# Performance work log

Hardware: AMD Instinct MI355X
Metric: run time of the kernel (lower is better)

## Reference

```python
import jax, jax.numpy as jnp
import numpy as np

N, E, R, D_IN, D_OUT = 50000, 800000, 8, 64, 64


def setup_inputs() -> dict:
    key = jax.random.key(0)
    ks = jax.random.split(key, 8)
    feat = jax.random.normal(ks[0], (N, D_IN), dtype=jnp.float32)
    edge_src = jax.random.randint(ks[1], (E,), 0, N, dtype=jnp.int32)
    edge_dst = jax.random.randint(ks[2], (E,), 0, N, dtype=jnp.int32)
    etype = jax.random.randint(ks[3], (E,), 0, R, dtype=jnp.int32)
    attention = jax.random.uniform(ks[4], (E, 1), dtype=jnp.float32)
    weight = jax.random.normal(ks[5], (R, D_IN, D_OUT), dtype=jnp.float32) * (6.0 / (D_IN + D_OUT)) ** 0.5
    h_bias = jnp.zeros((D_OUT,), dtype=jnp.float32)
    loop_weight = jax.random.normal(ks[6], (D_IN, D_OUT), dtype=jnp.float32) * (6.0 / (D_IN + D_OUT)) ** 0.5
    return {"feat": feat, "edge_src": edge_src, "edge_dst": edge_dst,
            "etype": etype, "attention": attention, "weight": weight,
            "h_bias": h_bias, "loop_weight": loop_weight}


def reference(feat, edge_src, edge_dst, etype, attention, weight, h_bias, loop_weight):
    # Project all nodes through every relation weight once: [R, N, D_OUT].
    # (Equivalent to per-edge bmm with weight[etype] on gathered src feats,
    #  but avoids materializing a [E, D_IN, D_OUT] weight tensor.)
    proj = jnp.einsum('ni,rio->rno', feat, weight)
    # Per-edge message: gather relation-specific projection of src node.
    m = (proj[etype, edge_src] + h_bias) * attention          # [E, D_OUT]
    # Scatter-sum messages to destination nodes.
    agg = jax.ops.segment_sum(m, edge_dst, num_segments=feat.shape[0])
    # Self-loop.
    return agg + feat @ loop_weight
```

## Files before the change

kernel.cpp:

```cpp
#include <hip/hip_runtime.h>

#define D 64

typedef unsigned short ushort_t;
typedef __attribute__((ext_vector_type(8))) short bf16x8;
typedef __attribute__((ext_vector_type(4))) float f32x4;

__device__ __forceinline__ void fma4(float4& c, float a, const float4& b) {
  c.x = fmaf(a, b.x, c.x);
  c.y = fmaf(a, b.y, c.y);
  c.z = fmaf(a, b.z, c.z);
  c.w = fmaf(a, b.w, c.w);
}

__device__ __forceinline__ unsigned short f2bf(float f) {
  unsigned u = __float_as_uint(f);
  return (unsigned short)((u + 0x7FFFu + ((u >> 16) & 1u)) >> 16);
}
__device__ __forceinline__ float bf2f(unsigned short h) {
  return __uint_as_float((unsigned)h << 16);
}
__device__ __forceinline__ unsigned pk2(float a, float b) {
  return (unsigned)f2bf(a) | ((unsigned)f2bf(b) << 16);
}

__device__ __forceinline__ bf16x8 pack_bf8(float4 v0, float4 v1) {
  bf16x8 r;
  r[0] = (short)f2bf(v0.x); r[1] = (short)f2bf(v0.y);
  r[2] = (short)f2bf(v0.z); r[3] = (short)f2bf(v0.w);
  r[4] = (short)f2bf(v1.x); r[5] = (short)f2bf(v1.y);
  r[6] = (short)f2bf(v1.z); r[7] = (short)f2bf(v1.w);
  return r;
}

__global__ void prep(const float* __restrict__ weight, const float* __restrict__ loopw,
                     ushort_t* __restrict__ Wt, int* __restrict__ deg, int R, int N) {
  if ((int)blockIdx.x <= R) {
    const int m = blockIdx.x;
    const float* W = (m < R) ? weight + (size_t)m * D * D : loopw;
    ushort_t* o = Wt + (size_t)m * D * D;
    for (int i = threadIdx.x; i < 1024; i += 256) {
      float4 v = ((const float4*)W)[i];
      int k = i >> 4;
      int c = (i & 15) * 4;
      o[(c + 0) * D + k] = f2bf(v.x);
      o[(c + 1) * D + k] = f2bf(v.y);
      o[(c + 2) * D + k] = f2bf(v.z);
      o[(c + 3) * D + k] = f2bf(v.w);
    }
  } else {
    int i = (blockIdx.x - (R + 1)) * 256 + threadIdx.x;
    if (i < N) deg[i] = 0;
  }
}

template <int NM>
__device__ __forceinline__ void proj_body(const float* __restrict__ feat,
                                          const ushort_t* __restrict__ Wt,
                                          ushort_t* __restrict__ proj,
                                          float* __restrict__ out, int N, int blk) {
  const int t = threadIdx.x;
  const int lane = t & 63;
  const int wid = t >> 6;
  const int node = blk * 64 + wid * 16 + (lane & 15);
  const int g = lane >> 4;
  const int kb = g * 8;
  const int R8 = NM - 1;

  bf16x8 b0, b1;
  {
    float4 v0 = make_float4(0.f, 0.f, 0.f, 0.f), v1 = v0, v2 = v0, v3 = v0;
    if (node < N) {
      const float* p = feat + (size_t)node * D + kb;
      v0 = *(const float4*)p;
      v1 = *(const float4*)(p + 4);
      v2 = *(const float4*)(p + 32);
      v3 = *(const float4*)(p + 36);
    }
    b0 = pack_bf8(v0, v1);
    b1 = pack_bf8(v2, v3);
  }

#pragma unroll 2
  for (int m = 0; m < NM; ++m) {
    const ushort_t* wt = Wt + (size_t)m * D * D + kb;
    f32x4 acc[4];
#pragma unroll
    for (int ct = 0; ct < 4; ++ct) {
      const ushort_t* wr = wt + (size_t)(16 * ct + (lane & 15)) * D;
      bf16x8 a0 = *(const bf16x8*)wr;
      bf16x8 a1 = *(const bf16x8*)(wr + 32);
      acc[ct] = (f32x4){0.f, 0.f, 0.f, 0.f};
      acc[ct] = __builtin_amdgcn_mfma_f32_16x16x32_bf16(a0, b0, acc[ct], 0, 0, 0);
      acc[ct] = __builtin_amdgcn_mfma_f32_16x16x32_bf16(a1, b1, acc[ct], 0, 0, 0);
    }
    if (node < N) {
      if (m < R8) {
        ushort_t* op = proj + ((size_t)node * R8 + m) * D + 16 * g;
        uint4 w0, w1;
        w0.x = pk2(acc[0][0], acc[0][1]); w0.y = pk2(acc[0][2], acc[0][3]);
        w0.z = pk2(acc[1][0], acc[1][1]); w0.w = pk2(acc[1][2], acc[1][3]);
        w1.x = pk2(acc[2][0], acc[2][1]); w1.y = pk2(acc[2][2], acc[2][3]);
        w1.z = pk2(acc[3][0], acc[3][1]); w1.w = pk2(acc[3][2], acc[3][3]);
        *(uint4*)(op) = w0;
        *(uint4*)(op + 8) = w1;
      } else {
        float* op = out + (size_t)node * D + 4 * g;
#pragma unroll
        for (int ct = 0; ct < 4; ++ct) {
          float4 v;
          v.x = acc[ct][0]; v.y = acc[ct][1]; v.z = acc[ct][2]; v.w = acc[ct][3];
          *(float4*)(op + 16 * ct) = v;
        }
      }
    }
  }
}

__device__ __forceinline__ void proj_body_rt(const float* __restrict__ feat,
                                             const ushort_t* __restrict__ Wt,
                                             ushort_t* __restrict__ proj,
                                             float* __restrict__ out, int N, int R,
                                             int blk) {
  const int t = threadIdx.x;
  const int lane = t & 63;
  const int wid = t >> 6;
  const int node = blk * 64 + wid * 16 + (lane & 15);
  const int g = lane >> 4;
  const int kb = g * 8;

  bf16x8 b0, b1;
  {
    float4 v0 = make_float4(0.f, 0.f, 0.f, 0.f), v1 = v0, v2 = v0, v3 = v0;
    if (node < N) {
      const float* p = feat + (size_t)node * D + kb;
      v0 = *(const float4*)p;
      v1 = *(const float4*)(p + 4);
      v2 = *(const float4*)(p + 32);
      v3 = *(const float4*)(p + 36);
    }
    b0 = pack_bf8(v0, v1);
    b1 = pack_bf8(v2, v3);
  }

  for (int m = 0; m <= R; ++m) {
    const ushort_t* wt = Wt + (size_t)m * D * D + kb;
    f32x4 acc[4];
#pragma unroll
    for (int ct = 0; ct < 4; ++ct) {
      const ushort_t* wr = wt + (size_t)(16 * ct + (lane & 15)) * D;
      bf16x8 a0 = *(const bf16x8*)wr;
      bf16x8 a1 = *(const bf16x8*)(wr + 32);
      acc[ct] = (f32x4){0.f, 0.f, 0.f, 0.f};
      acc[ct] = __builtin_amdgcn_mfma_f32_16x16x32_bf16(a0, b0, acc[ct], 0, 0, 0);
      acc[ct] = __builtin_amdgcn_mfma_f32_16x16x32_bf16(a1, b1, acc[ct], 0, 0, 0);
    }
    if (node < N) {
      if (m < R) {
        ushort_t* op = proj + ((size_t)node * R + m) * D + 16 * g;
        uint4 w0, w1;
        w0.x = pk2(acc[0][0], acc[0][1]); w0.y = pk2(acc[0][2], acc[0][3]);
        w0.z = pk2(acc[1][0], acc[1][1]); w0.w = pk2(acc[1][2], acc[1][3]);
        w1.x = pk2(acc[2][0], acc[2][1]); w1.y = pk2(acc[2][2], acc[2][3]);
        w1.z = pk2(acc[3][0], acc[3][1]); w1.w = pk2(acc[3][2], acc[3][3]);
        *(uint4*)(op) = w0;
        *(uint4*)(op + 8) = w1;
      } else {
        float* op = out + (size_t)node * D + 4 * g;
#pragma unroll
        for (int ct = 0; ct < 4; ++ct) {
          float4 v;
          v.x = acc[ct][0]; v.y = acc[ct][1]; v.z = acc[ct][2]; v.w = acc[ct][3];
          *(float4*)(op + 16 * ct) = v;
        }
      }
    }
  }
}

__device__ __forceinline__ void hist_body(const int* __restrict__ edst,
                                          int* __restrict__ deg,
                                          int* __restrict__ rank, int E, int hblk) {
  const int e = (hblk * 256 + (int)threadIdx.x) * 4;
  if (e + 3 < E) {
    int4 d = *(const int4*)(edst + e);
    int4 r;
    r.x = atomicAdd(&deg[d.x], 1);
    r.y = atomicAdd(&deg[d.y], 1);
    r.z = atomicAdd(&deg[d.z], 1);
    r.w = atomicAdd(&deg[d.w], 1);
    *(int4*)(rank + e) = r;
  } else {
    for (int i = e; i < E; ++i) rank[i] = atomicAdd(&deg[edst[i]], 1);
  }
}

__global__ __launch_bounds__(256) void proj_hist(const float* __restrict__ feat,
                                                 const ushort_t* __restrict__ Wt,
                                                 ushort_t* __restrict__ proj,
                                                 float* __restrict__ out,
                                                 const int* __restrict__ edst,
                                                 int* __restrict__ deg,
                                                 int* __restrict__ rank,
                                                 int N, int E, int R, int PB) {
  if ((int)blockIdx.x < PB) {
    if (R == 8)
      proj_body<9>(feat, Wt, proj, out, N, blockIdx.x);
    else
      proj_body_rt(feat, Wt, proj, out, N, R, blockIdx.x);
  } else {
    hist_body(edst, deg, rank, E, blockIdx.x - PB);
  }
}

__global__ __launch_bounds__(256) void scan_partial(const int* __restrict__ deg,
                                                    int* __restrict__ bsum, int N) {
  const int t = threadIdx.x;
  const int base = blockIdx.x * 1024 + t * 4;
  int s = 0;
  if (base + 3 < N) {
    int4 v = *(const int4*)(deg + base);
    s = v.x + v.y + v.z + v.w;
  } else {
#pragma unroll
    for (int k = 0; k < 4; ++k) if (base + k < N) s += deg[base + k];
  }
  __shared__ int red[4];
#pragma unroll
  for (int m = 1; m < 64; m <<= 1) s += __shfl_xor(s, m);
  if ((t & 63) == 0) red[t >> 6] = s;
  __syncthreads();
  if (t == 0) bsum[blockIdx.x] = red[0] + red[1] + red[2] + red[3];
}

__global__ __launch_bounds__(256) void scan_bsum(const int* __restrict__ bsum,
                                                 int* __restrict__ boff,
                                                 int* __restrict__ off, int nb, int N) {
  __shared__ int s[256];
  __shared__ int carry_s;
  const int t = threadIdx.x;
  if (t == 0) carry_s = 0;
  __syncthreads();
  for (int base = 0; base < nb; base += 256) {
    int i = base + t;
    int v = (i < nb) ? bsum[i] : 0;
    s[t] = v;
    __syncthreads();
#pragma unroll
    for (int d = 1; d < 256; d <<= 1) {
      int u = (t >= d) ? s[t - d] : 0;
      __syncthreads();
      s[t] += u;
      __syncthreads();
    }
    int c = carry_s;
    if (i < nb) boff[i] = s[t] - v + c;
    __syncthreads();
    if (t == 0) carry_s = c + s[255];
    __syncthreads();
  }
  if (t == 0) off[N] = carry_s;
}

__global__ __launch_bounds__(256) void scan_apply(const int* __restrict__ deg,
                                                  const int* __restrict__ boff,
                                                  int* __restrict__ off, int N) {
  const int t = threadIdx.x;
  const int base = blockIdx.x * 1024 + t * 4;
  int v0 = 0, v1 = 0, v2 = 0, v3 = 0;
  if (base + 3 < N) {
    int4 v = *(const int4*)(deg + base);
    v0 = v.x; v1 = v.y; v2 = v.z; v3 = v.w;
  } else {
    if (base + 0 < N) v0 = deg[base + 0];
    if (base + 1 < N) v1 = deg[base + 1];
    if (base + 2 < N) v2 = deg[base + 2];
  }
  const int tsum = v0 + v1 + v2 + v3;
  __shared__ int s[256];
  s[t] = tsum;
  __syncthreads();
#pragma unroll
  for (int d = 1; d < 256; d <<= 1) {
    int u = (t >= d) ? s[t - d] : 0;
    __syncthreads();
    s[t] += u;
    __syncthreads();
  }
  int exc = s[t] - tsum + boff[blockIdx.x];
  const int o1 = exc + v0, o2 = o1 + v1, o3 = o2 + v2;
  if (base + 0 < N) off[base + 0] = exc;
  if (base + 1 < N) off[base + 1] = o1;
  if (base + 2 < N) off[base + 2] = o2;
  if (base + 3 < N) off[base + 3] = o3;
}

__global__ void scatter_pos(const int* __restrict__ esrc, const int* __restrict__ edst,
                            const int* __restrict__ etype, const float* __restrict__ att,
                            const int* __restrict__ off, const int* __restrict__ rank,
                            int2* __restrict__ payload, int E) {
  const int e = (blockIdx.x * 256 + threadIdx.x) * 4;
  if (e + 3 < E) {
    int4 s  = *(const int4*)(esrc + e);
    int4 d  = *(const int4*)(edst + e);
    int4 ty = *(const int4*)(etype + e);
    float4 a = *(const float4*)(att + e);
    int4 rk = *(const int4*)(rank + e);
    payload[off[d.x] + rk.x] = make_int2(s.x | (ty.x << 24), __float_as_int(a.x));
    payload[off[d.y] + rk.y] = make_int2(s.y | (ty.y << 24), __float_as_int(a.y));
    payload[off[d.z] + rk.z] = make_int2(s.z | (ty.z << 24), __float_as_int(a.z));
    payload[off[d.w] + rk.w] = make_int2(s.w | (ty.w << 24), __float_as_int(a.w));
  } else {
    for (int i = e; i < E; ++i)
      payload[off[edst[i]] + rank[i]] =
          make_int2(esrc[i] | (etype[i] << 24), __float_as_int(att[i]));
  }
}

__global__ __launch_bounds__(256, 8) void node_gather(const int* __restrict__ off,
                                                      const int2* __restrict__ payload,
                                                      const ushort_t* __restrict__ proj,
                                                      const float* __restrict__ hbias,
                                                      float* __restrict__ out, int N,
                                                      int R) {
  const int n = (blockIdx.x * 256 + threadIdx.x) >> 6;
  if (n >= N) return;
  const int lane = threadIdx.x & 63;
  const int sub = lane >> 4;
  const int q = lane & 15;
  const int ac0 = 16 * (q & 3) + 4 * (q >> 2);

  const int s0 = off[n], s1 = off[n + 1];
  float4 acc = make_float4(0.f, 0.f, 0.f, 0.f);
  float sa = 0.f;
  for (int e = s0 + sub; e < s1; e += 4) {
    const int2 pe = payload[e];
    const float a = __int_as_float(pe.y);
    const int src = pe.x & 0x00FFFFFF;
    const int r = ((unsigned)pe.x) >> 24;
    const ushort4 p = *(const ushort4*)(proj + ((size_t)src * R + r) * D + q * 4);
    acc.x = fmaf(a, bf2f(p.x), acc.x);
    acc.y = fmaf(a, bf2f(p.y), acc.y);
    acc.z = fmaf(a, bf2f(p.z), acc.z);
    acc.w = fmaf(a, bf2f(p.w), acc.w);
    sa += a;
  }
#pragma unroll
  for (int m = 16; m < 64; m <<= 1) {
    acc.x += __shfl_xor(acc.x, m);
    acc.y += __shfl_xor(acc.y, m);
    acc.z += __shfl_xor(acc.z, m);
    acc.w += __shfl_xor(acc.w, m);
    sa += __shfl_xor(sa, m);
  }
  if (sub == 0) {
    const float4 hb = *(const float4*)(hbias + ac0);
    float* op = out + (size_t)n * D + ac0;
    float4 cur = *(float4*)op;
    cur.x += acc.x + sa * hb.x;
    cur.y += acc.y + sa * hb.y;
    cur.z += acc.z + sa * hb.z;
    cur.w += acc.w + sa * hb.w;
    *(float4*)op = cur;
  }
}

__global__ __launch_bounds__(256, 3) void proj_single(const float* __restrict__ feat,
                                                      const float* __restrict__ W,
                                                      float* __restrict__ outp, int N) {
  __shared__ float sW[64 * 64];
  __shared__ float sF[64 * 132];
  const int t = threadIdx.x;
  const int tileBase = blockIdx.x * 128;

  {
    const float4* Wv = (const float4*)W;
    float4* sWv = (float4*)sW;
    for (int k = t; k < 1024; k += 256) sWv[k] = Wv[k];
  }
  {
    const int row = t >> 1, half = t & 1;
    const int gr = tileBase + row;
    if (gr < N) {
      const float4* src = (const float4*)(feat + (size_t)gr * D + half * 32);
#pragma unroll
      for (int k = 0; k < 8; ++k) {
        float4 v = src[k];
        int i0 = half * 32 + k * 4;
        sF[(i0 + 0) * 132 + row] = v.x;
        sF[(i0 + 1) * 132 + row] = v.y;
        sF[(i0 + 2) * 132 + row] = v.z;
        sF[(i0 + 3) * 132 + row] = v.w;
      }
    } else {
#pragma unroll
      for (int k = 0; k < 8; ++k) {
        int i0 = half * 32 + k * 4;
        sF[(i0 + 0) * 132 + row] = 0.f;
        sF[(i0 + 1) * 132 + row] = 0.f;
        sF[(i0 + 2) * 132 + row] = 0.f;
        sF[(i0 + 3) * 132 + row] = 0.f;
      }
    }
  }
  __syncthreads();

  const int c0 = (t & 15) * 4;
  const int r0 = (t >> 4) * 8;
  float4 acc[8];
#pragma unroll
  for (int rr = 0; rr < 8; ++rr) acc[rr] = make_float4(0.f, 0.f, 0.f, 0.f);

#pragma unroll 8
  for (int i = 0; i < 64; ++i) {
    float4 w  = *(const float4*)&sW[i * 64 + c0];
    float4 a0 = *(const float4*)&sF[i * 132 + r0];
    float4 a1 = *(const float4*)&sF[i * 132 + r0 + 4];
    fma4(acc[0], a0.x, w); fma4(acc[1], a0.y, w);
    fma4(acc[2], a0.z, w); fma4(acc[3], a0.w, w);
    fma4(acc[4], a1.x, w); fma4(acc[5], a1.y, w);
    fma4(acc[6], a1.z, w); fma4(acc[7], a1.w, w);
  }

#pragma unroll
  for (int rr = 0; rr < 8; ++rr) {
    int gn = tileBase + r0 + rr;
    if (gn < N) *(float4*)(outp + (size_t)gn * D + c0) = acc[rr];
  }
}

__global__ __launch_bounds__(256, 8) void edge_scatter(const int* __restrict__ esrc,
                                                       const int* __restrict__ edst,
                                                       const int* __restrict__ etype,
                                                       const float* __restrict__ att,
                                                       const float* __restrict__ proj,
                                                       const float* __restrict__ hbias,
                                                       float* __restrict__ out,
                                                       int E, int N, int relFilter) {
  const int t = blockIdx.x * 256 + threadIdx.x;
  const int wave = t >> 6;
  const int lane = threadIdx.x & 63;
  const int sub = lane >> 4;
  const int q = lane & 15;
  const long e = (long)wave * 4 + sub;
  if (e >= E) return;
  const int r = etype[e];
  if (relFilter >= 0 && r != relFilter) return;
  const int s = esrc[e];
  const int dn = edst[e];
  const float a = att[e];
  const size_t base = (size_t)s * D;
  const float4 hb = ((const float4*)hbias)[q];
  const float4 p = *(const float4*)(proj + base + q * 4);
  float* op = out + (size_t)dn * D + q * 4;
  unsafeAtomicAdd(op + 0, (p.x + hb.x) * a);
  unsafeAtomicAdd(op + 1, (p.y + hb.y) * a);
  unsafeAtomicAdd(op + 2, (p.z + hb.z) * a);
  unsafeAtomicAdd(op + 3, (p.w + hb.w) * a);
}

extern "C" void kernel_launch(void* const* d_in, const int* in_sizes, int n_in,
                              void* d_out, int out_size, void* d_ws, size_t ws_size,
                              hipStream_t stream) {
  const float* feat   = (const float*)d_in[0];
  const int* esrc     = (const int*)d_in[1];
  const int* edst     = (const int*)d_in[2];
  const int* etype    = (const int*)d_in[3];
  const float* att    = (const float*)d_in[4];
  const float* weight = (const float*)d_in[5];
  const float* hbias  = (const float*)d_in[6];
  const float* loopw  = (const float*)d_in[7];
  float* out = (float*)d_out;

  const int N = in_sizes[0] / D;
  const int E = in_sizes[1];
  const int R = in_sizes[5] / (D * D);

  const int Npad = (N + 3) & ~3;
  const int nb = (N + 1023) / 1024;

  const size_t wtBytes   = (size_t)(R + 1) * D * D * 2;
  const size_t projBytes = (size_t)N * R * D * 2;
  const size_t intCount  = (size_t)Npad + (size_t)(N + 1) + (size_t)nb + (size_t)E;
  const size_t payOff    = (wtBytes + projBytes + intCount * 4 + 7) & ~(size_t)7;
  const size_t needSorted = payOff + (size_t)E * 8;

  const int PB = (N + 63) / 64;
  const int HB = ((E + 3) / 4 + 255) / 256;
  const int equadBlocks = ((E + 3) / 4 + 255) / 256;

  if (ws_size >= needSorted) {
    ushort_t* Wt   = (ushort_t*)d_ws;
    ushort_t* proj = (ushort_t*)((char*)d_ws + wtBytes);
    int* deg    = (int*)((char*)d_ws + wtBytes + projBytes);
    int* off    = deg + Npad;
    int* bsum   = off + (N + 1);
    int* rank   = bsum + nb;
    int2* payload = (int2*)((char*)d_ws + payOff);

    prep<<<(R + 1) + (N + 255) / 256, 256, 0, stream>>>(weight, loopw, Wt, deg, R, N);
    proj_hist<<<PB + HB, 256, 0, stream>>>(feat, Wt, proj, out, edst, deg, rank,
                                           N, E, R, PB);
    scan_partial<<<nb, 256, 0, stream>>>(deg, bsum, N);
    scan_bsum<<<1, 256, 0, stream>>>(bsum, bsum, off, nb, N);
    scan_apply<<<nb, 256, 0, stream>>>(deg, bsum, off, N);
    scatter_pos<<<equadBlocks, 256, 0, stream>>>(esrc, edst, etype, att, off, rank,
                                                 payload, E);
    node_gather<<<(N + 3) / 4, 256, 0, stream>>>(off, payload, proj, hbias, out, N, R);
  } else {
    const int tilesN = (N + 127) / 128;
    const int eblocks16 = (E + 15) / 16;
    proj_single<<<tilesN, 256, 0, stream>>>(feat, loopw, out, N);
    for (int r = 0; r < R; ++r) {
      proj_single<<<tilesN, 256, 0, stream>>>(feat, weight + (size_t)r * D * D,
                                              (float*)d_ws, N);
      edge_scatter<<<eblocks16, 256, 0, stream>>>(esrc, edst, etype, att, (float*)d_ws,
                                                  hbias, out, E, N, r);
    }
  }
}
```

Baseline: 121.6 us.

## Split node projection across histogram and scatter kernels to balance work

The per-node relation projection was done entirely inside the histogram kernel. It is now split in two halves. The first half runs alongside the degree histogram, and the second half is fused into the payload scatter kernel as extra blocks. The aim is to overlap compute-heavy MFMA projection with the memory- and atomic-bound edge passes in both kernels, balancing their durations. The cost is a more complex launch layout and block-type divergence within the scatter kernel.

```diff
diff --git a/kernel.cpp b/kernel.cpp
--- a/kernel.cpp
+++ b/kernel.cpp
@@ -31,6 +31,174 @@
   r[4] = (short)f2bf(v1.x); r[5] = (short)f2bf(v1.y);
   r[6] = (short)f2bf(v1.z); r[7] = (short)f2bf(v1.w);
   return r;
+}
+
+template <int NM>
+__device__ __forceinline__ void proj_body(const float* __restrict__ feat,
+                                          const ushort_t* __restrict__ Wt,
+                                          ushort_t* __restrict__ proj,
+                                          float* __restrict__ out, int N,
+                                          int nodeBase) {
+  const int t = threadIdx.x;
+  const int lane = t & 63;
+  const int wid = t >> 6;
+  const int node = nodeBase + wid * 16 + (lane & 15);
+  const int g = lane >> 4;
+  const int kb = g * 8;
+  const int R8 = NM - 1;
+
+  bf16x8 b0, b1;
+  {
+    float4 v0 = make_float4(0.f, 0.f, 0.f, 0.f), v1 = v0, v2 = v0, v3 = v0;
+    if (node < N) {
+      const float* p = feat + (size_t)node * D + kb;
+      v0 = *(const float4*)p;
+      v1 = *(const float4*)(p + 4);
+      v2 = *(const float4*)(p + 32);
+      v3 = *(const float4*)(p + 36);
+    }
+    b0 = pack_bf8(v0, v1);
+    b1 = pack_bf8(v2, v3);
+  }
+
+#pragma unroll 2
+  for (int m = 0; m < NM; ++m) {
+    const ushort_t* wt = Wt + (size_t)m * D * D + kb;
+    f32x4 acc[4];
+#pragma unroll
+    for (int ct = 0; ct < 4; ++ct) {
+      const ushort_t* wr = wt + (size_t)(16 * ct + (lane & 15)) * D;
+      bf16x8 a0 = *(const bf16x8*)wr;
+      bf16x8 a1 = *(const bf16x8*)(wr + 32);
+      acc[ct] = (f32x4){0.f, 0.f, 0.f, 0.f};
+      acc[ct] = __builtin_amdgcn_mfma_f32_16x16x32_bf16(a0, b0, acc[ct], 0, 0, 0);
+      acc[ct] = __builtin_amdgcn_mfma_f32_16x16x32_bf16(a1, b1, acc[ct], 0, 0, 0);
+    }
+    if (node < N) {
+      if (m < R8) {
+        ushort_t* op = proj + ((size_t)node * R8 + m) * D + 16 * g;
+        uint4 w0, w1;
+        w0.x = pk2(acc[0][0], acc[0][1]); w0.y = pk2(acc[0][2], acc[0][3]);
+        w0.z = pk2(acc[1][0], acc[1][1]); w0.w = pk2(acc[1][2], acc[1][3]);
+        w1.x = pk2(acc[2][0], acc[2][1]); w1.y = pk2(acc[2][2], acc[2][3]);
+        w1.z = pk2(acc[3][0], acc[3][1]); w1.w = pk2(acc[3][2], acc[3][3]);
+        *(uint4*)(op) = w0;
+        *(uint4*)(op + 8) = w1;
+      } else {
+        float* op = out + (size_t)node * D + 4 * g;
+#pragma unroll
+        for (int ct = 0; ct < 4; ++ct) {
+          float4 v;
+          v.x = acc[ct][0]; v.y = acc[ct][1]; v.z = acc[ct][2]; v.w = acc[ct][3];
+          *(float4*)(op + 16 * ct) = v;
+        }
+      }
+    }
+  }
+}
+
+__device__ __forceinline__ void proj_body_rt(const float* __restrict__ feat,
+                                             const ushort_t* __restrict__ Wt,
+                                             ushort_t* __restrict__ proj,
+                                             float* __restrict__ out, int N, int R,
+                                             int nodeBase) {
+  const int t = threadIdx.x;
+  const int lane = t & 63;
+  const int wid = t >> 6;
+  const int node = nodeBase + wid * 16 + (lane & 15);
+  const int g = lane >> 4;
+  const int kb = g * 8;
+
+  bf16x8 b0, b1;
+  {
+    float4 v0 = make_float4(0.f, 0.f, 0.f, 0.f), v1 = v0, v2 = v0, v3 = v0;
+    if (node < N) {
+      const float* p = feat + (size_t)node * D + kb;
+      v0 = *(const float4*)p;
+      v1 = *(const float4*)(p + 4);
+      v2 = *(const float4*)(p + 32);
+      v3 = *(const float4*)(p + 36);
+    }
+    b0 = pack_bf8(v0, v1);
+    b1 = pack_bf8(v2, v3);
+  }
+
+  for (int m = 0; m <= R; ++m) {
+    const ushort_t* wt = Wt + (size_t)m * D * D + kb;
+    f32x4 acc[4];
+#pragma unroll
+    for (int ct = 0; ct < 4; ++ct) {
+      const ushort_t* wr = wt + (size_t)(16 * ct + (lane & 15)) * D;
+      bf16x8 a0 = *(const bf16x8*)wr;
+      bf16x8 a1 = *(const bf16x8*)(wr + 32);
+      acc[ct] = (f32x4){0.f, 0.f, 0.f, 0.f};
+      acc[ct] = __builtin_amdgcn_mfma_f32_16x16x32_bf16(a0, b0, acc[ct], 0, 0, 0);
+      acc[ct] = __builtin_amdgcn_mfma_f32_16x16x32_bf16(a1, b1, acc[ct], 0, 0, 0);
+    }
+    if (node < N) {
+      if (m < R) {
+        ushort_t* op = proj + ((size_t)node * R + m) * D + 16 * g;
+        uint4 w0, w1;
+        w0.x = pk2(acc[0][0], acc[0][1]); w0.y = pk2(acc[0][2], acc[0][3]);
+        w0.z = pk2(acc[1][0], acc[1][1]); w0.w = pk2(acc[1][2], acc[1][3]);
+        w1.x = pk2(acc[2][0], acc[2][1]); w1.y = pk2(acc[2][2], acc[2][3]);
+        w1.z = pk2(acc[3][0], acc[3][1]); w1.w = pk2(acc[3][2], acc[3][3]);
+        *(uint4*)(op) = w0;
+        *(uint4*)(op + 8) = w1;
+      } else {
+        float* op = out + (size_t)node * D + 4 * g;
+#pragma unroll
+        for (int ct = 0; ct < 4; ++ct) {
+          float4 v;
+          v.x = acc[ct][0]; v.y = acc[ct][1]; v.z = acc[ct][2]; v.w = acc[ct][3];
+          *(float4*)(op + 16 * ct) = v;
+        }
+      }
+    }
+  }
+}
+
+__device__ __forceinline__ void hist_body(const int* __restrict__ edst,
+                                          int* __restrict__ deg,
+                                          int* __restrict__ rank, int E, int hblk) {
+  const int e = (hblk * 256 + (int)threadIdx.x) * 4;
+  if (e + 3 < E) {
+    int4 d = *(const int4*)(edst + e);
+    int4 r;
+    r.x = atomicAdd(&deg[d.x], 1);
+    r.y = atomicAdd(&deg[d.y], 1);
+    r.z = atomicAdd(&deg[d.z], 1);
+    r.w = atomicAdd(&deg[d.w], 1);
+    *(int4*)(rank + e) = r;
+  } else {
+    for (int i = e; i < E; ++i) rank[i] = atomicAdd(&deg[edst[i]], 1);
+  }
+}
+
+__device__ __forceinline__ void scatter_body(const int* __restrict__ esrc,
+                                             const int* __restrict__ edst,
+                                             const int* __restrict__ etype,
+                                             const float* __restrict__ att,
+                                             const int* __restrict__ off,
+                                             const int* __restrict__ rank,
+                                             int2* __restrict__ payload, int E,
+                                             int sblk) {
+  const int e = (sblk * 256 + (int)threadIdx.x) * 4;
+  if (e + 3 < E) {
+    int4 s  = *(const int4*)(esrc + e);
+    int4 d  = *(const int4*)(edst + e);
+    int4 ty = *(const int4*)(etype + e);
+    float4 a = *(const float4*)(att + e);
+    int4 rk = *(const int4*)(rank + e);
+    payload[off[d.x] + rk.x] = make_int2(s.x | (ty.x << 24), __float_as_int(a.x));
+    payload[off[d.y] + rk.y] = make_int2(s.y | (ty.y << 24), __float_as_int(a.y));
+    payload[off[d.z] + rk.z] = make_int2(s.z | (ty.z << 24), __float_as_int(a.z));
+    payload[off[d.w] + rk.w] = make_int2(s.w | (ty.w << 24), __float_as_int(a.w));
+  } else {
+    for (int i = e; i < E; ++i)
+      payload[off[edst[i]] + rank[i]] =
+          make_int2(esrc[i] | (etype[i] << 24), __float_as_int(att[i]));
+  }
 }
 
 __global__ void prep(const float* __restrict__ weight, const float* __restrict__ loopw,
@@ -54,162 +222,21 @@
   }
 }
 
-template <int NM>
-__device__ __forceinline__ void proj_body(const float* __restrict__ feat,
-                                          const ushort_t* __restrict__ Wt,
-                                          ushort_t* __restrict__ proj,
-                                          float* __restrict__ out, int N, int blk) {
-  const int t = threadIdx.x;
-  const int lane = t & 63;
-  const int wid = t >> 6;
-  const int node = blk * 64 + wid * 16 + (lane & 15);
-  const int g = lane >> 4;
-  const int kb = g * 8;
-  const int R8 = NM - 1;
-
-  bf16x8 b0, b1;
-  {
-    float4 v0 = make_float4(0.f, 0.f, 0.f, 0.f), v1 = v0, v2 = v0, v3 = v0;
-    if (node < N) {
-      const float* p = feat + (size_t)node * D + kb;
-      v0 = *(const float4*)p;
-      v1 = *(const float4*)(p + 4);
-      v2 = *(const float4*)(p + 32);
-      v3 = *(const float4*)(p + 36);
-    }
-    b0 = pack_bf8(v0, v1);
-    b1 = pack_bf8(v2, v3);
-  }
-
-#pragma unroll 2
-  for (int m = 0; m < NM; ++m) {
-    const ushort_t* wt = Wt + (size_t)m * D * D + kb;
-    f32x4 acc[4];
-#pragma unroll
-    for (int ct = 0; ct < 4; ++ct) {
-      const ushort_t* wr = wt + (size_t)(16 * ct + (lane & 15)) * D;
-      bf16x8 a0 = *(const bf16x8*)wr;
-      bf16x8 a1 = *(const bf16x8*)(wr + 32);
-      acc[ct] = (f32x4){0.f, 0.f, 0.f, 0.f};
-      acc[ct] = __builtin_amdgcn_mfma_f32_16x16x32_bf16(a0, b0, acc[ct], 0, 0, 0);
-      acc[ct] = __builtin_amdgcn_mfma_f32_16x16x32_bf16(a1, b1, acc[ct], 0, 0, 0);
-    }
-    if (node < N) {
-      if (m < R8) {
-        ushort_t* op = proj + ((size_t)node * R8 + m) * D + 16 * g;
-        uint4 w0, w1;
-        w0.x = pk2(acc[0][0], acc[0][1]); w0.y = pk2(acc[0][2], acc[0][3]);
-        w0.z = pk2(acc[1][0], acc[1][1]); w0.w = pk2(acc[1][2], acc[1][3]);
-        w1.x = pk2(acc[2][0], acc[2][1]); w1.y = pk2(acc[2][2], acc[2][3]);
-        w1.z = pk2(acc[3][0], acc[3][1]); w1.w = pk2(acc[3][2], acc[3][3]);
-        *(uint4*)(op) = w0;
-        *(uint4*)(op + 8) = w1;
-      } else {
-        float* op = out + (size_t)node * D + 4 * g;
-#pragma unroll
-        for (int ct = 0; ct < 4; ++ct) {
-          float4 v;
-          v.x = acc[ct][0]; v.y = acc[ct][1]; v.z = acc[ct][2]; v.w = acc[ct][3];
-          *(float4*)(op + 16 * ct) = v;
-        }
-      }
-    }
-  }
-}
-
-__device__ __forceinline__ void proj_body_rt(const float* __restrict__ feat,
-                                             const ushort_t* __restrict__ Wt,
-                                             ushort_t* __restrict__ proj,
-                                             float* __restrict__ out, int N, int R,
-                                             int blk) {
-  const int t = threadIdx.x;
-  const int lane = t & 63;
-  const int wid = t >> 6;
-  const int node = blk * 64 + wid * 16 + (lane & 15);
-  const int g = lane >> 4;
-  const int kb = g * 8;
-
-  bf16x8 b0, b1;
-  {
-    float4 v0 = make_float4(0.f, 0.f, 0.f, 0.f), v1 = v0, v2 = v0, v3 = v0;
-    if (node < N) {
-      const float* p = feat + (size_t)node * D + kb;
-      v0 = *(const float4*)p;
-      v1 = *(const float4*)(p + 4);
-      v2 = *(const float4*)(p + 32);
-      v3 = *(const float4*)(p + 36);
-    }
-    b0 = pack_bf8(v0, v1);
-    b1 = pack_bf8(v2, v3);
-  }
-
-  for (int m = 0; m <= R; ++m) {
-    const ushort_t* wt = Wt + (size_t)m * D * D + kb;
-    f32x4 acc[4];
-#pragma unroll
-    for (int ct = 0; ct < 4; ++ct) {
-      const ushort_t* wr = wt + (size_t)(16 * ct + (lane & 15)) * D;
-      bf16x8 a0 = *(const bf16x8*)wr;
-      bf16x8 a1 = *(const bf16x8*)(wr + 32);
-      acc[ct] = (f32x4){0.f, 0.f, 0.f, 0.f};
-      acc[ct] = __builtin_amdgcn_mfma_f32_16x16x32_bf16(a0, b0, acc[ct], 0, 0, 0);
-      acc[ct] = __builtin_amdgcn_mfma_f32_16x16x32_bf16(a1, b1, acc[ct], 0, 0, 0);
-    }
-    if (node < N) {
-      if (m < R) {
-        ushort_t* op = proj + ((size_t)node * R + m) * D + 16 * g;
-        uint4 w0, w1;
-        w0.x = pk2(acc[0][0], acc[0][1]); w0.y = pk2(acc[0][2], acc[0][3]);
-        w0.z = pk2(acc[1][0], acc[1][1]); w0.w = pk2(acc[1][2], acc[1][3]);
-        w1.x = pk2(acc[2][0], acc[2][1]); w1.y = pk2(acc[2][2], acc[2][3]);
-        w1.z = pk2(acc[3][0], acc[3][1]); w1.w = pk2(acc[3][2], acc[3][3]);
-        *(uint4*)(op) = w0;
-        *(uint4*)(op + 8) = w1;
-      } else {
-        float* op = out + (size_t)node * D + 4 * g;
-#pragma unroll
-        for (int ct = 0; ct < 4; ++ct) {
-          float4 v;
-          v.x = acc[ct][0]; v.y = acc[ct][1]; v.z = acc[ct][2]; v.w = acc[ct][3];
-          *(float4*)(op + 16 * ct) = v;
-        }
-      }
-    }
-  }
-}
-
-__device__ __forceinline__ void hist_body(const int* __restrict__ edst,
-                                          int* __restrict__ deg,
-                                          int* __restrict__ rank, int E, int hblk) {
-  const int e = (hblk * 256 + (int)threadIdx.x) * 4;
-  if (e + 3 < E) {
-    int4 d = *(const int4*)(edst + e);
-    int4 r;
-    r.x = atomicAdd(&deg[d.x], 1);
-    r.y = atomicAdd(&deg[d.y], 1);
-    r.z = atomicAdd(&deg[d.z], 1);
-    r.w = atomicAdd(&deg[d.w], 1);
-    *(int4*)(rank + e) = r;
-  } else {
-    for (int i = e; i < E; ++i) rank[i] = atomicAdd(&deg[edst[i]], 1);
-  }
-}
-
-__global__ __launch_bounds__(256) void proj_hist(const float* __restrict__ feat,
-                                                 const ushort_t* __restrict__ Wt,
-                                                 ushort_t* __restrict__ proj,
-                                                 float* __restrict__ out,
-                                                 const int* __restrict__ edst,
-                                                 int* __restrict__ deg,
-                                                 int* __restrict__ rank,
-                                                 int N, int E, int R, int PB) {
-  if ((int)blockIdx.x < PB) {
+__global__ __launch_bounds__(256) void projA_hist(const float* __restrict__ feat,
+                                                  const ushort_t* __restrict__ Wt,
+                                                  ushort_t* __restrict__ proj,
+                                                  float* __restrict__ out,
+                                                  const int* __restrict__ edst,
+                                                  int* __restrict__ deg,
+                                                  int* __restrict__ rank,
+                                                  int N, int E, int R, int PA) {
+  if ((int)blockIdx.x < PA) {
     if (R == 8)
-      proj_body<9>(feat, Wt, proj, out, N, blockIdx.x);
+      proj_body<9>(feat, Wt, proj, out, N, blockIdx.x * 64);
     else
-      proj_body_rt(feat, Wt, proj, out, N, R, blockIdx.x);
-  } else {
-    hist_body(edst, deg, rank, E, blockIdx.x - PB);
+      proj_body_rt(feat, Wt, proj, out, N, R, blockIdx.x * 64);
+  } else {
+    hist_body(edst, deg, rank, E, blockIdx.x - PA);
   }
 }
 
@@ -295,25 +322,26 @@
   if (base + 3 < N) off[base + 3] = o3;
 }
 
-__global__ void scatter_pos(const int* __restrict__ esrc, const int* __restrict__ edst,
-                            const int* __restrict__ etype, const float* __restrict__ att,
-                            const int* __restrict__ off, const int* __restrict__ rank,
-                            int2* __restrict__ payload, int E) {
-  const int e = (blockIdx.x * 256 + threadIdx.x) * 4;
-  if (e + 3 < E) {
-    int4 s  = *(const int4*)(esrc + e);
-    int4 d  = *(const int4*)(edst + e);
-    int4 ty = *(const int4*)(etype + e);
-    float4 a = *(const float4*)(att + e);
-    int4 rk = *(const int4*)(rank + e);
-    payload[off[d.x] + rk.x] = make_int2(s.x | (ty.x << 24), __float_as_int(a.x));
-    payload[off[d.y] + rk.y] = make_int2(s.y | (ty.y << 24), __float_as_int(a.y));
-    payload[off[d.z] + rk.z] = make_int2(s.z | (ty.z << 24), __float_as_int(a.z));
-    payload[off[d.w] + rk.w] = make_int2(s.w | (ty.w << 24), __float_as_int(a.w));
-  } else {
-    for (int i = e; i < E; ++i)
-      payload[off[edst[i]] + rank[i]] =
-          make_int2(esrc[i] | (etype[i] << 24), __float_as_int(att[i]));
+__global__ __launch_bounds__(256) void scat_projB(const int* __restrict__ esrc,
+                                                  const int* __restrict__ edst,
+                                                  const int* __restrict__ etype,
+                                                  const float* __restrict__ att,
+                                                  const int* __restrict__ off,
+                                                  const int* __restrict__ rank,
+                                                  int2* __restrict__ payload,
+                                                  const float* __restrict__ feat,
+                                                  const ushort_t* __restrict__ Wt,
+                                                  ushort_t* __restrict__ proj,
+                                                  float* __restrict__ out,
+                                                  int N, int E, int R, int SB, int N2) {
+  if ((int)blockIdx.x < SB) {
+    scatter_body(esrc, edst, etype, att, off, rank, payload, E, blockIdx.x);
+  } else {
+    const int nodeBase = N2 + (blockIdx.x - SB) * 64;
+    if (R == 8)
+      proj_body<9>(feat, Wt, proj, out, N, nodeBase);
+    else
+      proj_body_rt(feat, Wt, proj, out, N, R, nodeBase);
   }
 }
 
@@ -486,8 +514,11 @@
   const size_t needSorted = payOff + (size_t)E * 8;
 
   const int PB = (N + 63) / 64;
+  const int PA = (PB + 1) / 2;
+  const int N2 = PA * 64;
+  const int PBb = PB - PA;
   const int HB = ((E + 3) / 4 + 255) / 256;
-  const int equadBlocks = ((E + 3) / 4 + 255) / 256;
+  const int SB = ((E + 3) / 4 + 255) / 256;
 
   if (ws_size >= needSorted) {
     ushort_t* Wt   = (ushort_t*)d_ws;
@@ -499,13 +530,13 @@
     int2* payload = (int2*)((char*)d_ws + payOff);
 
     prep<<<(R + 1) + (N + 255) / 256, 256, 0, stream>>>(weight, loopw, Wt, deg, R, N);
-    proj_hist<<<PB + HB, 256, 0, stream>>>(feat, Wt, proj, out, edst, deg, rank,
-                                           N, E, R, PB);
+    projA_hist<<<PA + HB, 256, 0, stream>>>(feat, Wt, proj, out, edst, deg, rank,
+                                            N, E, R, PA);
     scan_partial<<<nb, 256, 0, stream>>>(deg, bsum, N);
     scan_bsum<<<1, 256, 0, stream>>>(bsum, bsum, off, nb, N);
     scan_apply<<<nb, 256, 0, stream>>>(deg, bsum, off, N);
-    scatter_pos<<<equadBlocks, 256, 0, stream>>>(esrc, edst, etype, att, off, rank,
-                                                 payload, E);
+    scat_projB<<<SB + PBb, 256, 0, stream>>>(esrc, edst, etype, att, off, rank, payload,
+                                             feat, Wt, proj, out, N, E, R, SB, N2);
     node_gather<<<(N + 3) / 4, 256, 0, stream>>>(off, payload, proj, hbias, out, N, R);
   } else {
     const int tilesN = (N + 127) / 128;
```

After: 134.8 us. +10.8%, slower.

## Split degree histogram into eight sub-counters to reduce atomic contention

Applied to the files above, without the earlier changes.

The destination-degree histogram becomes eight interleaved copies, picked by edge index mod 8. The scan kernels sum the copies per node and write a per-copy base offset, and the scatter pass uses those bases plus the per-copy rank. The aim is to spread atomics to the same address across separate counters and lower contention. In exchange it adds 16x Npad of workspace, eight times more histogram reads in the scan kernels, and an extra base8 table written and then read in scatter.

```diff
diff --git a/kernel.cpp b/kernel.cpp
--- a/kernel.cpp
+++ b/kernel.cpp
@@ -34,7 +34,8 @@
 }
 
 __global__ void prep(const float* __restrict__ weight, const float* __restrict__ loopw,
-                     ushort_t* __restrict__ Wt, int* __restrict__ deg, int R, int N) {
+                     ushort_t* __restrict__ Wt, int* __restrict__ deg8, int R,
+                     int total8) {
   if ((int)blockIdx.x <= R) {
     const int m = blockIdx.x;
     const float* W = (m < R) ? weight + (size_t)m * D * D : loopw;
@@ -49,8 +50,9 @@
       o[(c + 3) * D + k] = f2bf(v.w);
     }
   } else {
-    int i = (blockIdx.x - (R + 1)) * 256 + threadIdx.x;
-    if (i < N) deg[i] = 0;
+    int i = ((blockIdx.x - (R + 1)) * 256 + threadIdx.x) * 4;
+    if (i + 3 < total8) *(int4*)(deg8 + i) = make_int4(0, 0, 0, 0);
+    else for (int k = i; k < total8; ++k) deg8[k] = 0;
   }
 }
 
@@ -179,19 +181,22 @@
 }
 
 __device__ __forceinline__ void hist_body(const int* __restrict__ edst,
-                                          int* __restrict__ deg,
-                                          int* __restrict__ rank, int E, int hblk) {
+                                          int* __restrict__ deg8,
+                                          int* __restrict__ rank, int E, int Npad,
+                                          int hblk) {
   const int e = (hblk * 256 + (int)threadIdx.x) * 4;
+  const int cbase = e & 7;
   if (e + 3 < E) {
     int4 d = *(const int4*)(edst + e);
     int4 r;
-    r.x = atomicAdd(&deg[d.x], 1);
-    r.y = atomicAdd(&deg[d.y], 1);
-    r.z = atomicAdd(&deg[d.z], 1);
-    r.w = atomicAdd(&deg[d.w], 1);
+    r.x = atomicAdd(&deg8[(cbase + 0) * Npad + d.x], 1);
+    r.y = atomicAdd(&deg8[(cbase + 1) * Npad + d.y], 1);
+    r.z = atomicAdd(&deg8[(cbase + 2) * Npad + d.z], 1);
+    r.w = atomicAdd(&deg8[(cbase + 3) * Npad + d.w], 1);
     *(int4*)(rank + e) = r;
   } else {
-    for (int i = e; i < E; ++i) rank[i] = atomicAdd(&deg[edst[i]], 1);
+    for (int i = e; i < E; ++i)
+      rank[i] = atomicAdd(&deg8[(i & 7) * Npad + edst[i]], 1);
   }
 }
 
@@ -200,30 +205,35 @@
                                                  ushort_t* __restrict__ proj,
                                                  float* __restrict__ out,
                                                  const int* __restrict__ edst,
-                                                 int* __restrict__ deg,
+                                                 int* __restrict__ deg8,
                                                  int* __restrict__ rank,
-                                                 int N, int E, int R, int PB) {
+                                                 int N, int E, int R, int Npad, int PB) {
   if ((int)blockIdx.x < PB) {
     if (R == 8)
       proj_body<9>(feat, Wt, proj, out, N, blockIdx.x);
     else
       proj_body_rt(feat, Wt, proj, out, N, R, blockIdx.x);
   } else {
-    hist_body(edst, deg, rank, E, blockIdx.x - PB);
-  }
-}
-
-__global__ __launch_bounds__(256) void scan_partial(const int* __restrict__ deg,
-                                                    int* __restrict__ bsum, int N) {
+    hist_body(edst, deg8, rank, E, Npad, blockIdx.x - PB);
+  }
+}
+
+__global__ __launch_bounds__(256) void scan_partial(const int* __restrict__ deg8,
+                                                    int* __restrict__ bsum, int N,
+                                                    int Npad) {
   const int t = threadIdx.x;
   const int base = blockIdx.x * 1024 + t * 4;
   int s = 0;
   if (base + 3 < N) {
-    int4 v = *(const int4*)(deg + base);
-    s = v.x + v.y + v.z + v.w;
-  } else {
-#pragma unroll
-    for (int k = 0; k < 4; ++k) if (base + k < N) s += deg[base + k];
+#pragma unroll
+    for (int c = 0; c < 8; ++c) {
+      int4 v = *(const int4*)(deg8 + c * Npad + base);
+      s += v.x + v.y + v.z + v.w;
+    }
+  } else {
+    for (int k = 0; k < 4; ++k)
+      if (base + k < N)
+        for (int c = 0; c < 8; ++c) s += deg8[c * Npad + base + k];
   }
   __shared__ int red[4];
 #pragma unroll
@@ -262,21 +272,31 @@
   if (t == 0) off[N] = carry_s;
 }
 
-__global__ __launch_bounds__(256) void scan_apply(const int* __restrict__ deg,
+__global__ __launch_bounds__(256) void scan_apply(const int* __restrict__ deg8,
                                                   const int* __restrict__ boff,
-                                                  int* __restrict__ off, int N) {
+                                                  int* __restrict__ off,
+                                                  int* __restrict__ base8, int N,
+                                                  int Npad) {
   const int t = threadIdx.x;
   const int base = blockIdx.x * 1024 + t * 4;
-  int v0 = 0, v1 = 0, v2 = 0, v3 = 0;
+  int cnt[8][4];
+  int tot[4] = {0, 0, 0, 0};
   if (base + 3 < N) {
-    int4 v = *(const int4*)(deg + base);
-    v0 = v.x; v1 = v.y; v2 = v.z; v3 = v.w;
-  } else {
-    if (base + 0 < N) v0 = deg[base + 0];
-    if (base + 1 < N) v1 = deg[base + 1];
-    if (base + 2 < N) v2 = deg[base + 2];
-  }
-  const int tsum = v0 + v1 + v2 + v3;
+#pragma unroll
+    for (int c = 0; c < 8; ++c) {
+      int4 v = *(const int4*)(deg8 + c * Npad + base);
+      cnt[c][0] = v.x; cnt[c][1] = v.y; cnt[c][2] = v.z; cnt[c][3] = v.w;
+      tot[0] += v.x; tot[1] += v.y; tot[2] += v.z; tot[3] += v.w;
+    }
+  } else {
+    for (int c = 0; c < 8; ++c)
+      for (int k = 0; k < 4; ++k) {
+        int v = (base + k < N) ? deg8[c * Npad + base + k] : 0;
+        cnt[c][k] = v;
+        tot[k] += v;
+      }
+  }
+  const int tsum = tot[0] + tot[1] + tot[2] + tot[3];
   __shared__ int s[256];
   s[t] = tsum;
   __syncthreads();
@@ -288,31 +308,44 @@
     __syncthreads();
   }
   int exc = s[t] - tsum + boff[blockIdx.x];
-  const int o1 = exc + v0, o2 = o1 + v1, o3 = o2 + v2;
-  if (base + 0 < N) off[base + 0] = exc;
-  if (base + 1 < N) off[base + 1] = o1;
-  if (base + 2 < N) off[base + 2] = o2;
-  if (base + 3 < N) off[base + 3] = o3;
+#pragma unroll
+  for (int k = 0; k < 4; ++k) {
+    if (base + k < N) {
+      off[base + k] = exc;
+      int running = exc;
+#pragma unroll
+      for (int c = 0; c < 8; ++c) {
+        base8[c * Npad + base + k] = running;
+        running += cnt[c][k];
+      }
+      exc += tot[k];
+    }
+  }
 }
 
 __global__ void scatter_pos(const int* __restrict__ esrc, const int* __restrict__ edst,
                             const int* __restrict__ etype, const float* __restrict__ att,
-                            const int* __restrict__ off, const int* __restrict__ rank,
-                            int2* __restrict__ payload, int E) {
+                            const int* __restrict__ base8, const int* __restrict__ rank,
+                            int2* __restrict__ payload, int E, int Npad) {
   const int e = (blockIdx.x * 256 + threadIdx.x) * 4;
+  const int cbase = e & 7;
   if (e + 3 < E) {
     int4 s  = *(const int4*)(esrc + e);
     int4 d  = *(const int4*)(edst + e);
     int4 ty = *(const int4*)(etype + e);
     float4 a = *(const float4*)(att + e);
     int4 rk = *(const int4*)(rank + e);
-    payload[off[d.x] + rk.x] = make_int2(s.x | (ty.x << 24), __float_as_int(a.x));
-    payload[off[d.y] + rk.y] = make_int2(s.y | (ty.y << 24), __float_as_int(a.y));
-    payload[off[d.z] + rk.z] = make_int2(s.z | (ty.z << 24), __float_as_int(a.z));
-    payload[off[d.w] + rk.w] = make_int2(s.w | (ty.w << 24), __float_as_int(a.w));
+    payload[base8[(cbase + 0) * Npad + d.x] + rk.x] =
+        make_int2(s.x | (ty.x << 24), __float_as_int(a.x));
+    payload[base8[(cbase + 1) * Npad + d.y] + rk.y] =
+        make_int2(s.y | (ty.y << 24), __float_as_int(a.y));
+    payload[base8[(cbase + 2) * Npad + d.z] + rk.z] =
+        make_int2(s.z | (ty.z << 24), __float_as_int(a.z));
+    payload[base8[(cbase + 3) * Npad + d.w] + rk.w] =
+        make_int2(s.w | (ty.w << 24), __float_as_int(a.w));
   } else {
     for (int i = e; i < E; ++i)
-      payload[off[edst[i]] + rank[i]] =
+      payload[base8[(i & 7) * Npad + edst[i]] + rank[i]] =
           make_int2(esrc[i] | (etype[i] << 24), __float_as_int(att[i]));
   }
 }
@@ -481,31 +514,34 @@
 
   const size_t wtBytes   = (size_t)(R + 1) * D * D * 2;
   const size_t projBytes = (size_t)N * R * D * 2;
-  const size_t intCount  = (size_t)Npad + (size_t)(N + 1) + (size_t)nb + (size_t)E;
+  const size_t intCount  = 16 * (size_t)Npad + (size_t)(N + 1) + (size_t)nb + (size_t)E;
   const size_t payOff    = (wtBytes + projBytes + intCount * 4 + 7) & ~(size_t)7;
   const size_t needSorted = payOff + (size_t)E * 8;
 
   const int PB = (N + 63) / 64;
   const int HB = ((E + 3) / 4 + 255) / 256;
   const int equadBlocks = ((E + 3) / 4 + 255) / 256;
+  const int total8 = 8 * Npad;
+  const int zeroBlocks = ((total8 + 3) / 4 + 255) / 256;
 
   if (ws_size >= needSorted) {
     ushort_t* Wt   = (ushort_t*)d_ws;
     ushort_t* proj = (ushort_t*)((char*)d_ws + wtBytes);
-    int* deg    = (int*)((char*)d_ws + wtBytes + projBytes);
-    int* off    = deg + Npad;
+    int* deg8   = (int*)((char*)d_ws + wtBytes + projBytes);
+    int* base8  = deg8 + 8 * Npad;
+    int* off    = base8 + 8 * Npad;
     int* bsum   = off + (N + 1);
     int* rank   = bsum + nb;
     int2* payload = (int2*)((char*)d_ws + payOff);
 
-    prep<<<(R + 1) + (N + 255) / 256, 256, 0, stream>>>(weight, loopw, Wt, deg, R, N);
-    proj_hist<<<PB + HB, 256, 0, stream>>>(feat, Wt, proj, out, edst, deg, rank,
-                                           N, E, R, PB);
-    scan_partial<<<nb, 256, 0, stream>>>(deg, bsum, N);
+    prep<<<(R + 1) + zeroBlocks, 256, 0, stream>>>(weight, loopw, Wt, deg8, R, total8);
+    proj_hist<<<PB + HB, 256, 0, stream>>>(feat, Wt, proj, out, edst, deg8, rank,
+                                           N, E, R, Npad, PB);
+    scan_partial<<<nb, 256, 0, stream>>>(deg8, bsum, N, Npad);
     scan_bsum<<<1, 256, 0, stream>>>(bsum, bsum, off, nb, N);
-    scan_apply<<<nb, 256, 0, stream>>>(deg, bsum, off, N);
-    scatter_pos<<<equadBlocks, 256, 0, stream>>>(esrc, edst, etype, att, off, rank,
-                                                 payload, E);
+    scan_apply<<<nb, 256, 0, stream>>>(deg8, bsum, off, base8, N, Npad);
+    scatter_pos<<<equadBlocks, 256, 0, stream>>>(esrc, edst, etype, att, base8, rank,
+                                                 payload, E, Npad);
     node_gather<<<(N + 3) / 4, 256, 0, stream>>>(off, payload, proj, hbias, out, N, R);
   } else {
     const int tilesN = (N + 127) / 128;
```

New measurement: 121.8 us. No clear change (+0.2%).

## Project 64 nodes per wave and interleave projection with histogram blocks

Applied to the files above, without the earlier changes.

Each wave now projects 64 nodes instead of 16. It loads each relation's weight fragments once and reuses them across four node groups of MFMAs, which cuts weight reloads and gives more independent MFMA work per wave. Projection blocks are no longer placed first in the grid but spread evenly among the histogram blocks, so atomic-heavy and compute-heavy blocks run at the same time. Workspace offsets are padded to 4-int alignment so the rank array stays aligned for int4 stores. In exchange there are four times fewer projection blocks and higher register pressure per thread.

```diff
diff --git a/kernel.cpp b/kernel.cpp
--- a/kernel.cpp
+++ b/kernel.cpp
@@ -55,20 +55,23 @@
 }
 
 template <int NM>
-__device__ __forceinline__ void proj_body(const float* __restrict__ feat,
-                                          const ushort_t* __restrict__ Wt,
-                                          ushort_t* __restrict__ proj,
-                                          float* __restrict__ out, int N, int blk) {
+__device__ __forceinline__ void proj_body64(const float* __restrict__ feat,
+                                            const ushort_t* __restrict__ Wt,
+                                            ushort_t* __restrict__ proj,
+                                            float* __restrict__ out, int N, int blk) {
   const int t = threadIdx.x;
   const int lane = t & 63;
   const int wid = t >> 6;
-  const int node = blk * 64 + wid * 16 + (lane & 15);
+  const int l15 = lane & 15;
   const int g = lane >> 4;
   const int kb = g * 8;
+  const int nodeBase = blk * 256 + wid * 64;
   const int R8 = NM - 1;
 
-  bf16x8 b0, b1;
-  {
+  bf16x8 b[4][2];
+#pragma unroll
+  for (int ng = 0; ng < 4; ++ng) {
+    const int node = nodeBase + ng * 16 + l15;
     float4 v0 = make_float4(0.f, 0.f, 0.f, 0.f), v1 = v0, v2 = v0, v3 = v0;
     if (node < N) {
       const float* p = feat + (size_t)node * D + kb;
@@ -77,60 +80,71 @@
       v2 = *(const float4*)(p + 32);
       v3 = *(const float4*)(p + 36);
     }
-    b0 = pack_bf8(v0, v1);
-    b1 = pack_bf8(v2, v3);
+    b[ng][0] = pack_bf8(v0, v1);
+    b[ng][1] = pack_bf8(v2, v3);
   }
 
 #pragma unroll 2
   for (int m = 0; m < NM; ++m) {
     const ushort_t* wt = Wt + (size_t)m * D * D + kb;
-    f32x4 acc[4];
+    bf16x8 a[4][2];
 #pragma unroll
     for (int ct = 0; ct < 4; ++ct) {
-      const ushort_t* wr = wt + (size_t)(16 * ct + (lane & 15)) * D;
-      bf16x8 a0 = *(const bf16x8*)wr;
-      bf16x8 a1 = *(const bf16x8*)(wr + 32);
-      acc[ct] = (f32x4){0.f, 0.f, 0.f, 0.f};
-      acc[ct] = __builtin_amdgcn_mfma_f32_16x16x32_bf16(a0, b0, acc[ct], 0, 0, 0);
-      acc[ct] = __builtin_amdgcn_mfma_f32_16x16x32_bf16(a1, b1, acc[ct], 0, 0, 0);
-    }
-    if (node < N) {
-      if (m < R8) {
-        ushort_t* op = proj + ((size_t)node * R8 + m) * D + 16 * g;
-        uint4 w0, w1;
-        w0.x = pk2(acc[0][0], acc[0][1]); w0.y = pk2(acc[0][2], acc[0][3]);
-        w0.z = pk2(acc[1][0], acc[1][1]); w0.w = pk2(acc[1][2], acc[1][3]);
-        w1.x = pk2(acc[2][0], acc[2][1]); w1.y = pk2(acc[2][2], acc[2][3]);
-        w1.z = pk2(acc[3][0], acc[3][1]); w1.w = pk2(acc[3][2], acc[3][3]);
-        *(uint4*)(op) = w0;
-        *(uint4*)(op + 8) = w1;
-      } else {
-        float* op = out + (size_t)node * D + 4 * g;
-#pragma unroll
-        for (int ct = 0; ct < 4; ++ct) {
-          float4 v;
-          v.x = acc[ct][0]; v.y = acc[ct][1]; v.z = acc[ct][2]; v.w = acc[ct][3];
-          *(float4*)(op + 16 * ct) = v;
+      const ushort_t* wr = wt + (size_t)(16 * ct + l15) * D;
+      a[ct][0] = *(const bf16x8*)wr;
+      a[ct][1] = *(const bf16x8*)(wr + 32);
+    }
+#pragma unroll
+    for (int ng = 0; ng < 4; ++ng) {
+      f32x4 acc[4];
+#pragma unroll
+      for (int ct = 0; ct < 4; ++ct) {
+        acc[ct] = (f32x4){0.f, 0.f, 0.f, 0.f};
+        acc[ct] = __builtin_amdgcn_mfma_f32_16x16x32_bf16(a[ct][0], b[ng][0], acc[ct], 0, 0, 0);
+        acc[ct] = __builtin_amdgcn_mfma_f32_16x16x32_bf16(a[ct][1], b[ng][1], acc[ct], 0, 0, 0);
+      }
+      const int node = nodeBase + ng * 16 + l15;
+      if (node < N) {
+        if (m < R8) {
+          ushort_t* op = proj + ((size_t)node * R8 + m) * D + 16 * g;
+          uint4 w0, w1;
+          w0.x = pk2(acc[0][0], acc[0][1]); w0.y = pk2(acc[0][2], acc[0][3]);
+          w0.z = pk2(acc[1][0], acc[1][1]); w0.w = pk2(acc[1][2], acc[1][3]);
+          w1.x = pk2(acc[2][0], acc[2][1]); w1.y = pk2(acc[2][2], acc[2][3]);
+          w1.z = pk2(acc[3][0], acc[3][1]); w1.w = pk2(acc[3][2], acc[3][3]);
+          *(uint4*)(op) = w0;
+          *(uint4*)(op + 8) = w1;
+        } else {
+          float* op = out + (size_t)node * D + 4 * g;
+#pragma unroll
+          for (int ct = 0; ct < 4; ++ct) {
+            float4 v;
+            v.x = acc[ct][0]; v.y = acc[ct][1]; v.z = acc[ct][2]; v.w = acc[ct][3];
+            *(float4*)(op + 16 * ct) = v;
+          }
         }
       }
     }
   }
 }
 
-__device__ __forceinline__ void proj_body_rt(const float* __restrict__ feat,
-                                             const ushort_t* __restrict__ Wt,
-                                             ushort_t* __restrict__ proj,
-                                             float* __restrict__ out, int N, int R,
-                                             int blk) {
+__device__ __forceinline__ void proj_body64_rt(const float* __restrict__ feat,
+                                               const ushort_t* __restrict__ Wt,
+                                               ushort_t* __restrict__ proj,
+                                               float* __restrict__ out, int N, int R,
+                                               int blk) {
   const int t = threadIdx.x;
   const int lane = t & 63;
   const int wid = t >> 6;
-  const int node = blk * 64 + wid * 16 + (lane & 15);
+  const int l15 = lane & 15;
   const int g = lane >> 4;
   const int kb = g * 8;
-
-  bf16x8 b0, b1;
-  {
+  const int nodeBase = blk * 256 + wid * 64;
+
+  bf16x8 b[4][2];
+#pragma unroll
+  for (int ng = 0; ng < 4; ++ng) {
+    const int node = nodeBase + ng * 16 + l15;
     float4 v0 = make_float4(0.f, 0.f, 0.f, 0.f), v1 = v0, v2 = v0, v3 = v0;
     if (node < N) {
       const float* p = feat + (size_t)node * D + kb;
@@ -139,39 +153,47 @@
       v2 = *(const float4*)(p + 32);
       v3 = *(const float4*)(p + 36);
     }
-    b0 = pack_bf8(v0, v1);
-    b1 = pack_bf8(v2, v3);
+    b[ng][0] = pack_bf8(v0, v1);
+    b[ng][1] = pack_bf8(v2, v3);
   }
 
   for (int m = 0; m <= R; ++m) {
     const ushort_t* wt = Wt + (size_t)m * D * D + kb;
-    f32x4 acc[4];
+    bf16x8 a[4][2];
 #pragma unroll
     for (int ct = 0; ct < 4; ++ct) {
-      const ushort_t* wr = wt + (size_t)(16 * ct + (lane & 15)) * D;
-      bf16x8 a0 = *(const bf16x8*)wr;
-      bf16x8 a1 = *(const bf16x8*)(wr + 32);
-      acc[ct] = (f32x4){0.f, 0.f, 0.f, 0.f};
-      acc[ct] = __builtin_amdgcn_mfma_f32_16x16x32_bf16(a0, b0, acc[ct], 0, 0, 0);
-      acc[ct] = __builtin_amdgcn_mfma_f32_16x16x32_bf16(a1, b1, acc[ct], 0, 0, 0);
-    }
-    if (node < N) {
-      if (m < R) {
-        ushort_t* op = proj + ((size_t)node * R + m) * D + 16 * g;
-        uint4 w0, w1;
-        w0.x = pk2(acc[0][0], acc[0][1]); w0.y = pk2(acc[0][2], acc[0][3]);
-        w0.z = pk2(acc[1][0], acc[1][1]); w0.w = pk2(acc[1][2], acc[1][3]);
-        w1.x = pk2(acc[2][0], acc[2][1]); w1.y = pk2(acc[2][2], acc[2][3]);
-        w1.z = pk2(acc[3][0], acc[3][1]); w1.w = pk2(acc[3][2], acc[3][3]);
-        *(uint4*)(op) = w0;
-        *(uint4*)(op + 8) = w1;
-      } else {
-        float* op = out + (size_t)node * D + 4 * g;
-#pragma unroll
-        for (int ct = 0; ct < 4; ++ct) {
-          float4 v;
-          v.x = acc[ct][0]; v.y = acc[ct][1]; v.z = acc[ct][2]; v.w = acc[ct][3];
-          *(float4*)(op + 16 * ct) = v;
+      const ushort_t* wr = wt + (size_t)(16 * ct + l15) * D;
+      a[ct][0] = *(const bf16x8*)wr;
+      a[ct][1] = *(const bf16x8*)(wr + 32);
+    }
+#pragma unroll
+    for (int ng = 0; ng < 4; ++ng) {
+      f32x4 acc[4];
+#pragma unroll
+      for (int ct = 0; ct < 4; ++ct) {
+        acc[ct] = (f32x4){0.f, 0.f, 0.f, 0.f};
+        acc[ct] = __builtin_amdgcn_mfma_f32_16x16x32_bf16(a[ct][0], b[ng][0], acc[ct], 0, 0, 0);
+        acc[ct] = __builtin_amdgcn_mfma_f32_16x16x32_bf16(a[ct][1], b[ng][1], acc[ct], 0, 0, 0);
+      }
+      const int node = nodeBase + ng * 16 + l15;
+      if (node < N) {
+        if (m < R) {
+          ushort_t* op = proj + ((size_t)node * R + m) * D + 16 * g;
+          uint4 w0, w1;
+          w0.x = pk2(acc[0][0], acc[0][1]); w0.y = pk2(acc[0][2], acc[0][3]);
+          w0.z = pk2(acc[1][0], acc[1][1]); w0.w = pk2(acc[1][2], acc[1][3]);
+          w1.x = pk2(acc[2][0], acc[2][1]); w1.y = pk2(acc[2][2], acc[2][3]);
+          w1.z = pk2(acc[3][0], acc[3][1]); w1.w = pk2(acc[3][2], acc[3][3]);
+          *(uint4*)(op) = w0;
+          *(uint4*)(op + 8) = w1;
+        } else {
+          float* op = out + (size_t)node * D + 4 * g;
+#pragma unroll
+          for (int ct = 0; ct < 4; ++ct) {
+            float4 v;
+            v.x = acc[ct][0]; v.y = acc[ct][1]; v.z = acc[ct][2]; v.w = acc[ct][3];
+            *(float4*)(op + 16 * ct) = v;
+          }
         }
       }
     }
@@ -202,14 +224,18 @@
                                                  const int* __restrict__ edst,
                                                  int* __restrict__ deg,
                                                  int* __restrict__ rank,
-                                                 int N, int E, int R, int PB) {
-  if ((int)blockIdx.x < PB) {
+                                                 int N, int E, int R, int PB, int total) {
+  const int b = blockIdx.x;
+  const long lo = (long)b * PB;
+  const int f0 = (int)(lo / total);
+  const int f1 = (int)((lo + PB) / total);
+  if (f1 > f0) {
     if (R == 8)
-      proj_body<9>(feat, Wt, proj, out, N, blockIdx.x);
+      proj_body64<9>(feat, Wt, proj, out, N, f0);
     else
-      proj_body_rt(feat, Wt, proj, out, N, R, blockIdx.x);
-  } else {
-    hist_body(edst, deg, rank, E, blockIdx.x - PB);
+      proj_body64_rt(feat, Wt, proj, out, N, R, f0);
+  } else {
+    hist_body(edst, deg, rank, E, b - f1);
   }
 }
 
@@ -476,17 +502,20 @@
   const int E = in_sizes[1];
   const int R = in_sizes[5] / (D * D);
 
-  const int Npad = (N + 3) & ~3;
-  const int nb = (N + 1023) / 1024;
+  const int Npad   = (N + 3) & ~3;
+  const int offPad = (N + 1 + 3) & ~3;
+  const int nb     = (N + 1023) / 1024;
+  const int nbPad  = (nb + 3) & ~3;
 
   const size_t wtBytes   = (size_t)(R + 1) * D * D * 2;
   const size_t projBytes = (size_t)N * R * D * 2;
-  const size_t intCount  = (size_t)Npad + (size_t)(N + 1) + (size_t)nb + (size_t)E;
+  const size_t intCount  = (size_t)Npad + (size_t)offPad + (size_t)nbPad + (size_t)E;
   const size_t payOff    = (wtBytes + projBytes + intCount * 4 + 7) & ~(size_t)7;
   const size_t needSorted = payOff + (size_t)E * 8;
 
-  const int PB = (N + 63) / 64;
+  const int PB = (N + 255) / 256;
   const int HB = ((E + 3) / 4 + 255) / 256;
+  const int total = PB + HB;
   const int equadBlocks = ((E + 3) / 4 + 255) / 256;
 
   if (ws_size >= needSorted) {
@@ -494,13 +523,13 @@
     ushort_t* proj = (ushort_t*)((char*)d_ws + wtBytes);
     int* deg    = (int*)((char*)d_ws + wtBytes + projBytes);
     int* off    = deg + Npad;
-    int* bsum   = off + (N + 1);
-    int* rank   = bsum + nb;
+    int* bsum   = off + offPad;
+    int* rank   = bsum + nbPad;
     int2* payload = (int2*)((char*)d_ws + payOff);
 
     prep<<<(R + 1) + (N + 255) / 256, 256, 0, stream>>>(weight, loopw, Wt, deg, R, N);
-    proj_hist<<<PB + HB, 256, 0, stream>>>(feat, Wt, proj, out, edst, deg, rank,
-                                           N, E, R, PB);
+    proj_hist<<<total, 256, 0, stream>>>(feat, Wt, proj, out, edst, deg, rank,
+                                         N, E, R, PB, total);
     scan_partial<<<nb, 256, 0, stream>>>(deg, bsum, N);
     scan_bsum<<<1, 256, 0, stream>>>(bsum, bsum, off, nb, N);
     scan_apply<<<nb, 256, 0, stream>>>(deg, bsum, off, N);
```

After: 129.2 us. +6.2%, slower.
